# Kernel tuning notes

Measured on AMD Instinct MI355X. Metric: run time of the kernel, lower is better.

The kernel has to match this reference:

```python
import jax, jax.numpy as jnp
import numpy as np
jax.config.update("jax_enable_x64", True)

PRIMES = [2654435761, 2246822519, 3266489917, 2028178513, 1220703125, 1610612741, 805306457, 402653189, 3674653429, 2860486313, 1073676287, 2971215073, 1500450271, 3267000013, 2654435789, 4049292737]
WINDOWS = [1, 2, 4, 8]
BUCKETS = 2000000
SIGN_BITS = 8
BOUNDARY = 2
OFFSETS = (1, 2, 3, 4, 5, 6, 7, 8)
CHUNK = 32


def layer_norm(x, w, b, eps=1e-5):
    m = jnp.mean(x, axis=-1, keepdims=True)
    v = jnp.var(x, axis=-1, keepdims=True)
    return (x - m) * jax.lax.rsqrt(v + eps) * w + b


def shift_right(tokens, off):
    T = tokens.shape[1]
    return jnp.pad(tokens, ((0, 0), (off, 0)))[:, :T]


def hash_scale(tokens, window):
    # rolling polynomial hash: XOR of prime-multiplied shifted tokens
    h = jnp.zeros_like(tokens)
    for i in range(window):
        off = i + 1
        if off >= tokens.shape[1]:
            continue
        h = h ^ (shift_right(tokens, off) * PRIMES[i % len(PRIMES)])
    return h % BUCKETS


def tiny_scan(x, gw, gb, iw, ib, ow, ob, lnw, lnb):
    # chunked cumsum-based linear recurrence h_t = a_t * h_{t-1} + (1-a_t) * u_t
    B, T, D = x.shape
    S = gw.shape[0]
    K = min(CHUNK, T)
    g = jax.nn.sigmoid(jnp.einsum('btd,sd->bts', x, gw) + gb)
    drive = (1.0 - g) * (jnp.einsum('btd,sd->bts', x, iw) + ib)
    nC = T // K  # T chosen divisible by CHUNK
    a = g.reshape(B, nC, K, S)
    b = drive.reshape(B, nC, K, S)
    log_a = jnp.log(jnp.maximum(a, 1e-6))
    cum_a = jnp.exp(jnp.cumsum(log_a, axis=2))             # [B,nC,K,S]
    inv_cum_a = 1.0 / jnp.maximum(cum_a, 1e-8)
    cum_wb = jnp.cumsum(b * inv_cum_a, axis=2)

    def step(h, cs):
        ca, cw = cs                                        # [B,K,S]
        out = ca * (h[:, None, :] + cw)
        return out[:, -1], out

    h0 = jnp.zeros((B, S), x.dtype)
    _, outs = jax.lax.scan(step, h0, (jnp.swapaxes(cum_a, 0, 1), jnp.swapaxes(cum_wb, 0, 1)))
    states = jnp.swapaxes(outs, 0, 1).reshape(B, T, S)
    y = jnp.einsum('bts,ds->btd', states, ow) + ob
    return layer_norm(x + y, lnw, lnb)


def forward(chars, byte_embed, table0, table1, table2, table3, cond_w, conv_w, conv_b,
            gate_w, gate_b, inpr_w, inpr_b, outpr_w, outpr_b, scan_ln_w, scan_ln_b,
            inp_w, inp_b, r_w1, r_w2, r_proj, r_ln_w, r_ln_b, out_w, out_b):
    tokens = chars.astype(jnp.int64)
    B, T = tokens.shape
    tables = [table0, table1, table2, table3]
    keys = [hash_scale(tokens, WINDOWS[s]) for s in range(4)]
    short = [tables[s][keys[s]] for s in range(BOUNDARY)]     # each [B,T,2]
    # condition long-scale keys on sign bits of short-scale features
    cond_logits = jnp.einsum('btd,sd->bts', jnp.concatenate(short, axis=-1), cond_w)
    bits = (cond_logits > 0).astype(jnp.int64)                # [B,T,8]
    cond_key = jnp.zeros((B, T), dtype=jnp.int64)
    for i in range(SIGN_BITS):
        cond_key = cond_key ^ (bits[..., i] * PRIMES[i])
    longe = [tables[s][(keys[s] ^ cond_key) % BUCKETS] for s in range(BOUNDARY, 4)]
    hash_feat = jnp.concatenate(short + longe, axis=-1)       # [B,T,8]
    # causal depthwise conv over hash features
    C = hash_feat.shape[-1]
    ht = jnp.swapaxes(hash_feat, 1, 2)                        # [B,C,T]
    Kc = conv_w.shape[-1]
    conv = jax.lax.conv_general_dilated(ht, conv_w, (1,), [(Kc - 1, 0)],
                                        dimension_numbers=('NCH', 'OIH', 'NCH'),
                                        feature_group_count=C)
    hash_feat = jax.nn.silu(jnp.swapaxes(conv + conv_b[None, :, None], 1, 2))
    byte_emb = byte_embed[tokens]                             # [B,T,64]
    # match features: equality with k-shifted sequence
    mfs = []
    for k in OFFSETS:
        m = (tokens == shift_right(tokens, k)).astype(jnp.float32)
        m = m.at[:, :k].set(0.0)
        mfs.append(m)
    mf = jnp.stack(mfs, axis=-1)                              # [B,T,8]
    h = jnp.concatenate([byte_emb, hash_feat, mf], axis=-1)   # [B,T,80]
    h = tiny_scan(h, gate_w, gate_b, inpr_w, inpr_b, outpr_w, outpr_b, scan_ln_w, scan_ln_b)
    h = jax.nn.silu(jnp.einsum('btd,hd->bth', h, inp_w) + inp_b)   # [B,T,256]
    hh = jnp.einsum('bth,dh->btd',
                    jax.nn.silu(jnp.einsum('btd,hd->bth', h, r_w1)) * jnp.einsum('btd,hd->bth', h, r_w2),
                    r_proj)
    h = layer_norm(hh + h, r_ln_w, r_ln_b)
    return jnp.einsum('bth,vh->btv', h, out_w) + out_b        # [B,T,1024]


def setup_inputs() -> dict:
    key = jax.random.key(0)
    ks = jax.random.split(key, 32)
    f32 = jnp.float32
    B, T, V, EB, S, D, H = 32, 2048, 1024, 64, 32, 80, 256

    def rn(k, shape, std):
        return jax.random.normal(k, shape, dtype=f32) * std

    return {
        'chars': jax.random.randint(ks[0], (B, T), 0, V, dtype=jnp.int64),
        'byte_embed': rn(ks[1], (V, EB), 0.02),
        'table0': rn(ks[2], (BUCKETS, 2), 0.02),
        'table1': rn(ks[3], (BUCKETS, 2), 0.02),
        'table2': rn(ks[4], (BUCKETS, 2), 0.02),
        'table3': rn(ks[5], (BUCKETS, 2), 0.02),
        'cond_w': rn(ks[6], (SIGN_BITS, 2 * BOUNDARY), 0.3),
        'conv_w': rn(ks[7], (8, 1, 8), 0.2),
        'conv_b': rn(ks[8], (8,), 0.02),
        'gate_w': rn(ks[9], (S, D), 0.1),
        'gate_b': rn(ks[10], (S,), 0.02),
        'inpr_w': rn(ks[11], (S, D), 0.1),
        'inpr_b': rn(ks[12], (S,), 0.02),
        'outpr_w': rn(ks[13], (D, S), 0.1),
        'outpr_b': rn(ks[14], (D,), 0.02),
        'scan_ln_w': jnp.ones((D,), f32),
        'scan_ln_b': jnp.zeros((D,), f32),
        'inp_w': rn(ks[15], (H, D), 0.1),
        'inp_b': rn(ks[16], (H,), 0.02),
        'r_w1': rn(ks[17], (H, H), 0.05),
        'r_w2': rn(ks[18], (H, H), 0.05),
        'r_proj': rn(ks[19], (H, H), 0.05),
        'r_ln_w': jnp.ones((H,), f32),
        'r_ln_b': jnp.zeros((H,), f32),
        'out_w': rn(ks[20], (V, H), 0.05),
        'out_b': rn(ks[21], (V,), 0.02),
    }


def reference(chars, byte_embed, table0, table1, table2, table3, cond_w, conv_w, conv_b,
              gate_w, gate_b, inpr_w, inpr_b, outpr_w, outpr_b, scan_ln_w, scan_ln_b,
              inp_w, inp_b, r_w1, r_w2, r_proj, r_ln_w, r_ln_b, out_w, out_b):
    return forward(chars, byte_embed, table0, table1, table2, table3, cond_w, conv_w, conv_b,
                   gate_w, gate_b, inpr_w, inpr_b, outpr_w, outpr_b, scan_ln_w, scan_ln_b,
                   inp_w, inp_b, r_w1, r_w2, r_proj, r_ln_w, r_ln_b, out_w, out_b)
```

## Files before the change

kernel.cpp:

```cpp
#include <hip/hip_runtime.h>

#define BB 32
#define TT 2048
#define SS 32
#define DD 80
#define HH 256
#define VV 1024
#define EBD 64

typedef unsigned short u16;
typedef __attribute__((ext_vector_type(8))) __bf16 bf16x8;
typedef __attribute__((ext_vector_type(4))) float f32x4;

#define MFMA(a, b, c) __builtin_amdgcn_mfma_f32_16x16x32_bf16(a, b, c, 0, 0, 0)

__device__ inline u16 f2bu(float f) {
    unsigned u = __float_as_uint(f);
    return (u16)((u + 0x7FFFu + ((u >> 16) & 1u)) >> 16);
}
__device__ inline __bf16 f2b(float f) {
    u16 r = f2bu(f);
    return __builtin_bit_cast(__bf16, r);
}
__device__ inline float b2f(u16 h) { return __uint_as_float(((unsigned)h) << 16); }

__device__ inline bf16x8 ldfrag(const u16* base, int row, int k0, int lane) {
    return *(const bf16x8*)(base + (size_t)row * 256 + k0 + ((lane >> 4) << 3));
}
__device__ inline bf16x8 ldfrag96(const u16* base, int row, int k0, int lane) {
    return *(const bf16x8*)(base + (size_t)row * 96 + k0 + ((lane >> 4) << 3));
}

__global__ __launch_bounds__(256) void k_prep(const float* __restrict__ w1,
                                              const float* __restrict__ w2,
                                              const float* __restrict__ wp,
                                              const float* __restrict__ ow,
                                              const float* __restrict__ iw,
                                              u16* __restrict__ wbf) {
    int i = blockIdx.x * 256 + threadIdx.x;
    if (i >= 483328) return;
    float v;
    if (i < 65536) v = w1[i];
    else if (i < 131072) v = w2[i - 65536];
    else if (i < 196608) v = wp[i - 131072];
    else if (i < 458752) v = ow[i - 196608];
    else {
        int j = i - 458752;
        int row = j / 96, col = j % 96;
        v = (col < 80) ? iw[row * 80 + col] : 0.f;
    }
    wbf[i] = f2bu(v);
}

__global__ __launch_bounds__(256) void k_hash(const int* __restrict__ tok,
                                              const float* __restrict__ t0,
                                              const float* __restrict__ t1,
                                              const float* __restrict__ t2,
                                              const float* __restrict__ t3,
                                              const float* __restrict__ cond_w,
                                              float* __restrict__ raw) {
    int idx = blockIdx.x * 256 + threadIdx.x;
    if (idx >= BB * TT) return;
    int b = idx / TT, t = idx % TT;
    const int* tr = tok + b * TT;

    unsigned long long tv[8];
#pragma unroll
    for (int i = 0; i < 8; i++) {
        int ts = t - 1 - i;
        tv[i] = (ts >= 0) ? (unsigned long long)(unsigned)tr[ts] : 0ull;
    }
    const unsigned long long P[8] = {2654435761ull, 2246822519ull, 3266489917ull,
                                     2028178513ull, 1220703125ull, 1610612741ull,
                                     805306457ull, 402653189ull};
    unsigned long long x = 0ull;
    x ^= tv[0] * P[0]; unsigned long long k0 = x % 2000000ull;
    x ^= tv[1] * P[1]; unsigned long long k1 = x % 2000000ull;
    x ^= tv[2] * P[2]; x ^= tv[3] * P[3]; unsigned long long k2 = x % 2000000ull;
    x ^= tv[4] * P[4]; x ^= tv[5] * P[5];
    x ^= tv[6] * P[6]; x ^= tv[7] * P[7]; unsigned long long k3 = x % 2000000ull;

    float f0 = t0[k0 * 2], f1 = t0[k0 * 2 + 1];
    float f2 = t1[k1 * 2], f3 = t1[k1 * 2 + 1];

    unsigned long long ck = 0ull;
#pragma unroll
    for (int j = 0; j < 8; j++) {
        float lg = f0 * cond_w[j * 4 + 0] + f1 * cond_w[j * 4 + 1] +
                   f2 * cond_w[j * 4 + 2] + f3 * cond_w[j * 4 + 3];
        if (lg > 0.f) ck ^= P[j];
    }
    unsigned long long lk2 = (k2 ^ ck) % 2000000ull;
    unsigned long long lk3 = (k3 ^ ck) % 2000000ull;

    float* o = raw + (size_t)idx * 8;
    o[0] = f0; o[1] = f1; o[2] = f2; o[3] = f3;
    o[4] = t2[lk2 * 2]; o[5] = t2[lk2 * 2 + 1];
    o[6] = t3[lk3 * 2]; o[7] = t3[lk3 * 2 + 1];
}

__global__ __launch_bounds__(256) void k_feat(const int* __restrict__ tok,
                                              const float* __restrict__ be,
                                              const float* __restrict__ raw,
                                              const float* __restrict__ conv_w,
                                              const float* __restrict__ conv_b,
                                              float* __restrict__ hf) {
    int idx = blockIdx.x * 256 + threadIdx.x;
    if (idx >= BB * TT) return;
    int b = idx / TT, t = idx % TT;
    const int* tr = tok + b * TT;
    float* o = hf + (size_t)idx * DD;

    int tk = tr[t];
    const float* ber = be + (size_t)tk * EBD;
#pragma unroll
    for (int q = 0; q < 16; q++) *(f32x4*)(o + q * 4) = *(const f32x4*)(ber + q * 4);

#pragma unroll
    for (int c = 0; c < 8; c++) {
        float acc = conv_b[c];
#pragma unroll
        for (int k = 0; k < 8; k++) {
            int ts = t - 7 + k;
            if (ts >= 0) acc += conv_w[c * 8 + k] * raw[((size_t)(b * TT + ts)) * 8 + c];
        }
        o[64 + c] = acc / (1.f + expf(-acc));
    }

#pragma unroll
    for (int k = 1; k <= 8; k++) {
        float m = (t >= k && tk == tr[t - k]) ? 1.f : 0.f;
        o[71 + k] = m;
    }
}

__global__ __launch_bounds__(256) void k_gates(const float* __restrict__ hf,
                                               const float* __restrict__ gw,
                                               const float* __restrict__ gb,
                                               const float* __restrict__ iw,
                                               const float* __restrict__ ib,
                                               float* __restrict__ Ag,
                                               float* __restrict__ Dr) {
    __shared__ float xs[64][DD];
    __shared__ float gws[32 * 81];
    __shared__ float iws[32 * 81];
    int blk = blockIdx.x;
    int b = blk >> 5;
    int t0 = (blk & 31) << 6;
    const float* src = hf + ((size_t)(b * TT + t0)) * DD;
    for (int i = threadIdx.x; i < 64 * DD; i += 256) xs[i / DD][i % DD] = src[i];
    for (int i = threadIdx.x; i < 32 * 80; i += 256) {
        int s = i / 80, d = i % 80;
        gws[s * 81 + d] = gw[i];
        iws[s * 81 + d] = iw[i];
    }
    __syncthreads();

    for (int p = threadIdx.x; p < 64 * SS; p += 256) {
        int s = p & 31, tt = p >> 5;
        float ga = gb[s], ia = ib[s];
        for (int d = 0; d < DD; d++) {
            float xv = xs[tt][d];
            ga += xv * gws[s * 81 + d];
            ia += xv * iws[s * 81 + d];
        }
        float g = 1.f / (1.f + expf(-ga));
        float drv = (1.f - g) * ia;
        size_t oo = ((size_t)(b * SS + s)) * TT + t0 + tt;
        Ag[oo] = g;
        Dr[oo] = drv;
    }
}

__global__ __launch_bounds__(64) void k_scan_par(const float* __restrict__ Ag,
                                                 const float* __restrict__ Dr,
                                                 float* __restrict__ st) {
    int bs = blockIdx.x;
    int b = bs >> 5, s = bs & 31;
    int c = threadIdx.x;
    const float* ar = Ag + (size_t)bs * TT + c * 32;
    const float* dr = Dr + (size_t)bs * TT + c * 32;

    float ca[32], cw[32];
    float lacc = 0.f, wacc = 0.f;
#pragma unroll
    for (int k = 0; k < 32; k += 4) {
        f32x4 av = *(const f32x4*)(ar + k);
        f32x4 dv = *(const f32x4*)(dr + k);
#pragma unroll
        for (int j = 0; j < 4; j++) {
            lacc += logf(fmaxf(av[j], 1e-6f));
            float cav = expf(lacc);
            ca[k + j] = cav;
            wacc += dv[j] / fmaxf(cav, 1e-8f);
            cw[k + j] = wacc;
        }
    }

    float A = ca[31];
    float Bc = ca[31] * wacc;
    for (int off = 1; off < 64; off <<= 1) {
        float Ap = __shfl_up(A, off, 64);
        float Bp = __shfl_up(Bc, off, 64);
        if (c >= off) {
            Bc = A * Bp + Bc;
            A = A * Ap;
        }
    }
    float h0 = __shfl_up(Bc, 1, 64);
    if (c == 0) h0 = 0.f;

    float* op = st + ((size_t)(b * TT + c * 32)) * SS + s;
#pragma unroll
    for (int k = 0; k < 32; k++)
        op[(size_t)k * SS] = ca[k] * (h0 + cw[k]);
}

__global__ __launch_bounds__(256) void k_post(const float* __restrict__ st,
                                              const float* __restrict__ hf,
                                              const float* __restrict__ ow,
                                              const float* __restrict__ ob,
                                              const float* __restrict__ lnw,
                                              const float* __restrict__ lnb,
                                              u16* __restrict__ h1p) {
    __shared__ float ows[DD * SS];
    for (int i = threadIdx.x; i < DD * SS; i += 256) ows[i] = ow[i];
    __syncthreads();

    int idx = blockIdx.x * 256 + threadIdx.x;
    if (idx >= BB * TT) return;
    const float* sp = st + (size_t)idx * SS;
    float sv[SS];
#pragma unroll
    for (int i = 0; i < SS; i += 4) {
        f32x4 v4 = *(const f32x4*)(sp + i);
        sv[i] = v4[0]; sv[i + 1] = v4[1]; sv[i + 2] = v4[2]; sv[i + 3] = v4[3];
    }
    const float* x = hf + (size_t)idx * DD;

    float s1 = 0.f, s2 = 0.f;
    for (int d = 0; d < DD; d++) {
        float acc = ob[d];
#pragma unroll
        for (int i = 0; i < SS; i++) acc += sv[i] * ows[d * SS + i];
        float v = acc + x[d];
        s1 += v; s2 += v * v;
    }
    float m = s1 * (1.f / DD);
    float var = s2 * (1.f / DD) - m * m;
    float rs = rsqrtf(var + 1e-5f);
    u16* o = h1p + (size_t)idx * 96;
    for (int d = 0; d < DD; d++) {
        float acc = ob[d];
#pragma unroll
        for (int i = 0; i < SS; i++) acc += sv[i] * ows[d * SS + i];
        float v = acc + x[d];
        o[d] = f2bu((v - m) * rs * lnw[d] + lnb[d]);
    }
    *(f32x4*)(o + 80) = f32x4{0.f, 0.f, 0.f, 0.f};
    *(f32x4*)(o + 88) = f32x4{0.f, 0.f, 0.f, 0.f};
}

__global__ __launch_bounds__(256) void k_mlp1m(const u16* __restrict__ h1p,
                                               const u16* __restrict__ wb,
                                               const float* __restrict__ bias,
                                               u16* __restrict__ h2) {
    int lane = threadIdx.x & 63, wv = threadIdx.x >> 6;
    int r0 = blockIdx.x * 64;
    int c0 = wv * 64;
    f32x4 acc[4][4] = {};
#pragma unroll
    for (int ks = 0; ks < 3; ks++) {
        int k0 = ks * 32;
        bf16x8 a[4];
#pragma unroll
        for (int mi = 0; mi < 4; mi++) a[mi] = ldfrag96(h1p, r0 + mi * 16 + (lane & 15), k0, lane);
#pragma unroll
        for (int ni = 0; ni < 4; ni++) {
            bf16x8 b = ldfrag96(wb, c0 + ni * 16 + (lane & 15), k0, lane);
#pragma unroll
            for (int mi = 0; mi < 4; mi++) acc[mi][ni] = MFMA(a[mi], b, acc[mi][ni]);
        }
    }
    int g = lane >> 4, cl = lane & 15;
#pragma unroll
    for (int ni = 0; ni < 4; ni++) {
        float bv = bias[c0 + ni * 16 + cl];
#pragma unroll
        for (int mi = 0; mi < 4; mi++)
#pragma unroll
            for (int r = 0; r < 4; r++) {
                float v = acc[mi][ni][r] + bv;
                h2[(size_t)(r0 + mi * 16 + g * 4 + r) * 256 + c0 + ni * 16 + cl] =
                    f2bu(v / (1.f + expf(-v)));
            }
    }
}

__global__ __launch_bounds__(256) void k_gemm_u(const u16* __restrict__ x,
                                                const u16* __restrict__ w1,
                                                const u16* __restrict__ w2,
                                                u16* __restrict__ U) {
    int lane = threadIdx.x & 63, wv = threadIdx.x >> 6;
    int r0 = blockIdx.x * 64;
    int c0 = blockIdx.y * 128 + wv * 32;
    f32x4 a1[4][2] = {}, a2[4][2] = {};
    for (int ks = 0; ks < 8; ks++) {
        int k0 = ks * 32;
        bf16x8 a[4];
#pragma unroll
        for (int mi = 0; mi < 4; mi++) a[mi] = ldfrag(x, r0 + mi * 16 + (lane & 15), k0, lane);
#pragma unroll
        for (int ni = 0; ni < 2; ni++) {
            bf16x8 b1 = ldfrag(w1, c0 + ni * 16 + (lane & 15), k0, lane);
            bf16x8 b2 = ldfrag(w2, c0 + ni * 16 + (lane & 15), k0, lane);
#pragma unroll
            for (int mi = 0; mi < 4; mi++) {
                a1[mi][ni] = MFMA(a[mi], b1, a1[mi][ni]);
                a2[mi][ni] = MFMA(a[mi], b2, a2[mi][ni]);
            }
        }
    }
    int g = lane >> 4, cl = lane & 15;
#pragma unroll
    for (int mi = 0; mi < 4; mi++)
#pragma unroll
        for (int ni = 0; ni < 2; ni++)
#pragma unroll
            for (int r = 0; r < 4; r++) {
                float v1 = a1[mi][ni][r], v2 = a2[mi][ni][r];
                float u = v1 / (1.f + expf(-v1)) * v2;
                U[(size_t)(r0 + mi * 16 + g * 4 + r) * 256 + c0 + ni * 16 + cl] = f2bu(u);
            }
}

__global__ __launch_bounds__(256) void k_gemm_proj(const u16* __restrict__ U,
                                                   const u16* __restrict__ wp,
                                                   const u16* __restrict__ x,
                                                   const float* __restrict__ lnw,
                                                   const float* __restrict__ lnb,
                                                   u16* __restrict__ h3) {
    __shared__ float redS[64][4], redQ[64][4];
    int lane = threadIdx.x & 63, wv = threadIdx.x >> 6;
    int r0 = blockIdx.x * 64;
    int c0 = wv * 64;
    f32x4 acc[4][4] = {};
    for (int ks = 0; ks < 8; ks++) {
        int k0 = ks * 32;
        bf16x8 a[4];
#pragma unroll
        for (int mi = 0; mi < 4; mi++) a[mi] = ldfrag(U, r0 + mi * 16 + (lane & 15), k0, lane);
#pragma unroll
        for (int ni = 0; ni < 4; ni++) {
            bf16x8 b = ldfrag(wp, c0 + ni * 16 + (lane & 15), k0, lane);
#pragma unroll
            for (int mi = 0; mi < 4; mi++) acc[mi][ni] = MFMA(a[mi], b, acc[mi][ni]);
        }
    }
    int g = lane >> 4, cl = lane & 15;
#pragma unroll
    for (int mi = 0; mi < 4; mi++)
#pragma unroll
        for (int r = 0; r < 4; r++) {
            float s = 0.f, q = 0.f;
            int row = mi * 16 + g * 4 + r;
#pragma unroll
            for (int ni = 0; ni < 4; ni++) {
                int col = c0 + ni * 16 + cl;
                float v = acc[mi][ni][r] + b2f(x[(size_t)(r0 + row) * 256 + col]);
                acc[mi][ni][r] = v;
                s += v; q += v * v;
            }
            for (int m = 1; m < 16; m <<= 1) {
                s += __shfl_xor(s, m, 64);
                q += __shfl_xor(q, m, 64);
            }
            if (cl == 0) { redS[row][wv] = s; redQ[row][wv] = q; }
        }
    __syncthreads();

    float lw[4], lb[4];
#pragma unroll
    for (int ni = 0; ni < 4; ni++) {
        lw[ni] = lnw[c0 + ni * 16 + cl];
        lb[ni] = lnb[c0 + ni * 16 + cl];
    }
#pragma unroll
    for (int mi = 0; mi < 4; mi++)
#pragma unroll
        for (int r = 0; r < 4; r++) {
            int row = mi * 16 + g * 4 + r;
            float S = redS[row][0] + redS[row][1] + redS[row][2] + redS[row][3];
            float Q = redQ[row][0] + redQ[row][1] + redQ[row][2] + redQ[row][3];
            float m = S * (1.f / 256.f);
            float rs = rsqrtf(Q * (1.f / 256.f) - m * m + 1e-5f);
#pragma unroll
            for (int ni = 0; ni < 4; ni++) {
                float y = (acc[mi][ni][r] - m) * rs * lw[ni] + lb[ni];
                h3[(size_t)(r0 + row) * 256 + c0 + ni * 16 + cl] = f2bu(y);
            }
        }
}

#define SA 40
__global__ __launch_bounds__(256) void k_out3(const u16* __restrict__ h3,
                                              const u16* __restrict__ ow,
                                              const float* __restrict__ bias,
                                              float* __restrict__ out) {
    __shared__ u16 As[2][128 * SA];
    __shared__ u16 Bs[2][128 * SA];
    int tid = threadIdx.x, lane = tid & 63, wv = tid >> 6;
    int r0 = blockIdx.x * 128;
    int c0g = blockIdx.y * 128;
    int wr = (wv >> 1) * 64, wc = (wv & 1) * 64;
    int rl = lane & 15, g = lane >> 4;

    int row0_ = tid >> 2, cc0_ = tid & 3;
    int row1_ = (tid + 256) >> 2, cc1_ = tid & 3;
    bf16x8 rA0, rA1, rB0, rB1;

#define LOADT(kt)                                                                     \
    {                                                                                 \
        int kbase = (kt) * 32;                                                        \
        rA0 = *(const bf16x8*)(h3 + (size_t)(r0 + row0_) * 256 + kbase + cc0_ * 8);   \
        rA1 = *(const bf16x8*)(h3 + (size_t)(r0 + row1_) * 256 + kbase + cc1_ * 8);   \
        rB0 = *(const bf16x8*)(ow + (size_t)(c0g + row0_) * 256 + kbase + cc0_ * 8);  \
        rB1 = *(const bf16x8*)(ow + (size_t)(c0g + row1_) * 256 + kbase + cc1_ * 8);  \
    }
#define WRITET(buf)                                                                   \
    {                                                                                 \
        *(bf16x8*)&As[buf][row0_ * SA + cc0_ * 8] = rA0;                              \
        *(bf16x8*)&As[buf][row1_ * SA + cc1_ * 8] = rA1;                              \
        *(bf16x8*)&Bs[buf][row0_ * SA + cc0_ * 8] = rB0;                              \
        *(bf16x8*)&Bs[buf][row1_ * SA + cc1_ * 8] = rB1;                              \
    }

    LOADT(0);
    WRITET(0);
    f32x4 acc[4][4] = {};
    for (int kt = 0; kt < 8; kt++) {
        int buf = kt & 1;
        if (kt < 7) LOADT(kt + 1);
        __syncthreads();
        bf16x8 a[4], b[4];
#pragma unroll
        for (int mi = 0; mi < 4; mi++) a[mi] = *(const bf16x8*)&As[buf][(wr + mi * 16 + rl) * SA + g * 8];
#pragma unroll
        for (int ni = 0; ni < 4; ni++) b[ni] = *(const bf16x8*)&Bs[buf][(wc + ni * 16 + rl) * SA + g * 8];
#pragma unroll
        for (int ni = 0; ni < 4; ni++)
#pragma unroll
            for (int mi = 0; mi < 4; mi++) acc[mi][ni] = MFMA(a[mi], b[ni], acc[mi][ni]);
        if (kt < 7) WRITET(buf ^ 1);
    }
#undef LOADT
#undef WRITET

    int cl = lane & 15;
#pragma unroll
    for (int ni = 0; ni < 4; ni++) {
        float bv = bias[c0g + wc + ni * 16 + cl];
#pragma unroll
        for (int mi = 0; mi < 4; mi++)
#pragma unroll
            for (int r = 0; r < 4; r++)
                out[(size_t)(r0 + wr + mi * 16 + g * 4 + r) * VV + c0g + wc + ni * 16 + cl] =
                    acc[mi][ni][r] + bv;
    }
}

extern "C" void kernel_launch(void* const* d_in, const int* in_sizes, int n_in,
                              void* d_out, int out_size, void* d_ws, size_t ws_size,
                              hipStream_t stream) {
    const int* chars        = (const int*)d_in[0];
    const float* byte_embed = (const float*)d_in[1];
    const float* table0     = (const float*)d_in[2];
    const float* table1     = (const float*)d_in[3];
    const float* table2     = (const float*)d_in[4];
    const float* table3     = (const float*)d_in[5];
    const float* cond_w     = (const float*)d_in[6];
    const float* conv_w     = (const float*)d_in[7];
    const float* conv_b     = (const float*)d_in[8];
    const float* gate_w     = (const float*)d_in[9];
    const float* gate_b     = (const float*)d_in[10];
    const float* inpr_w     = (const float*)d_in[11];
    const float* inpr_b     = (const float*)d_in[12];
    const float* outpr_w    = (const float*)d_in[13];
    const float* outpr_b    = (const float*)d_in[14];
    const float* scan_ln_w  = (const float*)d_in[15];
    const float* scan_ln_b  = (const float*)d_in[16];
    const float* inp_w      = (const float*)d_in[17];
    const float* inp_b      = (const float*)d_in[18];
    const float* r_w1       = (const float*)d_in[19];
    const float* r_w2       = (const float*)d_in[20];
    const float* r_proj     = (const float*)d_in[21];
    const float* r_ln_w     = (const float*)d_in[22];
    const float* r_ln_b     = (const float*)d_in[23];
    const float* out_w      = (const float*)d_in[24];
    const float* out_b      = (const float*)d_in[25];

    char* ws = (char*)d_ws;
    u16*   wbf = (u16*)(ws + 0);
    u16*   w1b = wbf;
    u16*   w2b = wbf + 65536;
    u16*   wpb = wbf + 131072;
    u16*   owb = wbf + 196608;
    u16*   iwb = wbf + 458752;
    float* hf  = (float*)(ws + 1048576);
    float* raw = (float*)(ws + 24117248);
    float* Ag  = (float*)(ws + 24117248);
    float* Dr  = (float*)(ws + 32505856);
    float* st  = (float*)(ws + 40894464);
    u16*   h1p = (u16*)(ws + 49283072);
    u16*   h2b = (u16*)(ws + 1048576);
    u16*   Ub  = (u16*)(ws + 34603008);
    u16*   h3b = (u16*)(ws + 34603008);
    float* out = (float*)d_out;

    k_prep <<<1888, 256, 0, stream>>>(r_w1, r_w2, r_proj, out_w, inp_w, wbf);
    k_hash <<<256, 256, 0, stream>>>(chars, table0, table1, table2, table3, cond_w, raw);
    k_feat <<<256, 256, 0, stream>>>(chars, byte_embed, raw, conv_w, conv_b, hf);
    k_gates<<<1024, 256, 0, stream>>>(hf, gate_w, gate_b, inpr_w, inpr_b, Ag, Dr);
    k_scan_par<<<1024, 64, 0, stream>>>(Ag, Dr, st);
    k_post <<<256, 256, 0, stream>>>(st, hf, outpr_w, outpr_b, scan_ln_w, scan_ln_b, h1p);
    k_mlp1m<<<1024, 256, 0, stream>>>(h1p, iwb, inp_b, h2b);
    k_gemm_u   <<<dim3(1024, 2), 256, 0, stream>>>(h2b, w1b, w2b, Ub);
    k_gemm_proj<<<1024, 256, 0, stream>>>(Ub, wpb, h2b, r_ln_w, r_ln_b, h3b);
    k_out3     <<<dim3(512, 8), 256, 0, stream>>>(h3b, owb, out_b, out);
}
```

Before: 381.6 us.

## Fuse three MLP GEMMs into one kernel via LDS, loop output column groups

Merges the input projection, the gated SwiGLU GEMM and the projection+residual+layernorm kernel into one kernel per 64-row tile. Intermediates stay in shared memory instead of round-tripping through global memory. The output GEMM now loops over all 8 column groups inside each block instead of using a 2D grid, so the h3 tile is reused from cache. The cost is more LDS per block (about 68KB), which may lower occupancy, and the output grid shrinks to 512 blocks, each running longer.

```diff
diff --git a/kernel.cpp b/kernel.cpp
--- a/kernel.cpp
+++ b/kernel.cpp
@@ -261,149 +261,150 @@
     *(f32x4*)(o + 88) = f32x4{0.f, 0.f, 0.f, 0.f};
 }
 
-__global__ __launch_bounds__(256) void k_mlp1m(const u16* __restrict__ h1p,
-                                               const u16* __restrict__ wb,
-                                               const float* __restrict__ bias,
-                                               u16* __restrict__ h2) {
-    int lane = threadIdx.x & 63, wv = threadIdx.x >> 6;
-    int r0 = blockIdx.x * 64;
-    int c0 = wv * 64;
-    f32x4 acc[4][4] = {};
-#pragma unroll
-    for (int ks = 0; ks < 3; ks++) {
-        int k0 = ks * 32;
-        bf16x8 a[4];
-#pragma unroll
-        for (int mi = 0; mi < 4; mi++) a[mi] = ldfrag96(h1p, r0 + mi * 16 + (lane & 15), k0, lane);
-#pragma unroll
-        for (int ni = 0; ni < 4; ni++) {
-            bf16x8 b = ldfrag96(wb, c0 + ni * 16 + (lane & 15), k0, lane);
-#pragma unroll
-            for (int mi = 0; mi < 4; mi++) acc[mi][ni] = MFMA(a[mi], b, acc[mi][ni]);
-        }
-    }
-    int g = lane >> 4, cl = lane & 15;
-#pragma unroll
-    for (int ni = 0; ni < 4; ni++) {
-        float bv = bias[c0 + ni * 16 + cl];
-#pragma unroll
-        for (int mi = 0; mi < 4; mi++)
-#pragma unroll
-            for (int r = 0; r < 4; r++) {
-                float v = acc[mi][ni][r] + bv;
-                h2[(size_t)(r0 + mi * 16 + g * 4 + r) * 256 + c0 + ni * 16 + cl] =
-                    f2bu(v / (1.f + expf(-v)));
-            }
-    }
-}
-
-__global__ __launch_bounds__(256) void k_gemm_u(const u16* __restrict__ x,
+#define SX 264
+__global__ __launch_bounds__(256) void k_gmlp_f(const u16* __restrict__ h1p,
+                                                const u16* __restrict__ iwb,
+                                                const float* __restrict__ ibias,
                                                 const u16* __restrict__ w1,
                                                 const u16* __restrict__ w2,
-                                                u16* __restrict__ U) {
-    int lane = threadIdx.x & 63, wv = threadIdx.x >> 6;
-    int r0 = blockIdx.x * 64;
-    int c0 = blockIdx.y * 128 + wv * 32;
-    f32x4 a1[4][2] = {}, a2[4][2] = {};
-    for (int ks = 0; ks < 8; ks++) {
-        int k0 = ks * 32;
-        bf16x8 a[4];
-#pragma unroll
-        for (int mi = 0; mi < 4; mi++) a[mi] = ldfrag(x, r0 + mi * 16 + (lane & 15), k0, lane);
-#pragma unroll
-        for (int ni = 0; ni < 2; ni++) {
-            bf16x8 b1 = ldfrag(w1, c0 + ni * 16 + (lane & 15), k0, lane);
-            bf16x8 b2 = ldfrag(w2, c0 + ni * 16 + (lane & 15), k0, lane);
-#pragma unroll
-            for (int mi = 0; mi < 4; mi++) {
-                a1[mi][ni] = MFMA(a[mi], b1, a1[mi][ni]);
-                a2[mi][ni] = MFMA(a[mi], b2, a2[mi][ni]);
-            }
-        }
-    }
-    int g = lane >> 4, cl = lane & 15;
-#pragma unroll
-    for (int mi = 0; mi < 4; mi++)
-#pragma unroll
-        for (int ni = 0; ni < 2; ni++)
-#pragma unroll
-            for (int r = 0; r < 4; r++) {
-                float v1 = a1[mi][ni][r], v2 = a2[mi][ni][r];
-                float u = v1 / (1.f + expf(-v1)) * v2;
-                U[(size_t)(r0 + mi * 16 + g * 4 + r) * 256 + c0 + ni * 16 + cl] = f2bu(u);
-            }
-}
-
-__global__ __launch_bounds__(256) void k_gemm_proj(const u16* __restrict__ U,
-                                                   const u16* __restrict__ wp,
-                                                   const u16* __restrict__ x,
-                                                   const float* __restrict__ lnw,
-                                                   const float* __restrict__ lnb,
-                                                   u16* __restrict__ h3) {
+                                                const u16* __restrict__ wp,
+                                                const float* __restrict__ lnw,
+                                                const float* __restrict__ lnb,
+                                                u16* __restrict__ h3) {
+    __shared__ u16 Xs[64 * SX];
+    __shared__ u16 Us[64 * SX];
     __shared__ float redS[64][4], redQ[64][4];
     int lane = threadIdx.x & 63, wv = threadIdx.x >> 6;
     int r0 = blockIdx.x * 64;
-    int c0 = wv * 64;
-    f32x4 acc[4][4] = {};
-    for (int ks = 0; ks < 8; ks++) {
-        int k0 = ks * 32;
-        bf16x8 a[4];
-#pragma unroll
-        for (int mi = 0; mi < 4; mi++) a[mi] = ldfrag(U, r0 + mi * 16 + (lane & 15), k0, lane);
+    int g = lane >> 4, cl = lane & 15, rl = lane & 15;
+
+    {
+        int c0 = wv * 64;
+        f32x4 acc[4][4] = {};
+#pragma unroll
+        for (int ks = 0; ks < 3; ks++) {
+            int k0 = ks * 32;
+            bf16x8 a[4];
+#pragma unroll
+            for (int mi = 0; mi < 4; mi++) a[mi] = ldfrag96(h1p, r0 + mi * 16 + rl, k0, lane);
+#pragma unroll
+            for (int ni = 0; ni < 4; ni++) {
+                bf16x8 b = ldfrag96(iwb, c0 + ni * 16 + rl, k0, lane);
+#pragma unroll
+                for (int mi = 0; mi < 4; mi++) acc[mi][ni] = MFMA(a[mi], b, acc[mi][ni]);
+            }
+        }
 #pragma unroll
         for (int ni = 0; ni < 4; ni++) {
-            bf16x8 b = ldfrag(wp, c0 + ni * 16 + (lane & 15), k0, lane);
-#pragma unroll
-            for (int mi = 0; mi < 4; mi++) acc[mi][ni] = MFMA(a[mi], b, acc[mi][ni]);
-        }
-    }
-    int g = lane >> 4, cl = lane & 15;
-#pragma unroll
-    for (int mi = 0; mi < 4; mi++)
-#pragma unroll
-        for (int r = 0; r < 4; r++) {
-            float s = 0.f, q = 0.f;
-            int row = mi * 16 + g * 4 + r;
+            float bv = ibias[c0 + ni * 16 + cl];
+#pragma unroll
+            for (int mi = 0; mi < 4; mi++)
+#pragma unroll
+                for (int r = 0; r < 4; r++) {
+                    float v = acc[mi][ni][r] + bv;
+                    Xs[(mi * 16 + g * 4 + r) * SX + c0 + ni * 16 + cl] =
+                        f2bu(v / (1.f + expf(-v)));
+                }
+        }
+    }
+    __syncthreads();
+
+    for (int cg = 0; cg < 2; cg++) {
+        int c0 = cg * 128 + wv * 32;
+        f32x4 a1[4][2] = {}, a2[4][2] = {};
+        for (int ks = 0; ks < 8; ks++) {
+            int k0 = ks * 32 + (g << 3);
+            bf16x8 a[4];
+#pragma unroll
+            for (int mi = 0; mi < 4; mi++)
+                a[mi] = *(const bf16x8*)&Xs[(mi * 16 + rl) * SX + k0];
+#pragma unroll
+            for (int ni = 0; ni < 2; ni++) {
+                bf16x8 b1 = ldfrag(w1, c0 + ni * 16 + rl, ks * 32, lane);
+                bf16x8 b2 = ldfrag(w2, c0 + ni * 16 + rl, ks * 32, lane);
+#pragma unroll
+                for (int mi = 0; mi < 4; mi++) {
+                    a1[mi][ni] = MFMA(a[mi], b1, a1[mi][ni]);
+                    a2[mi][ni] = MFMA(a[mi], b2, a2[mi][ni]);
+                }
+            }
+        }
+#pragma unroll
+        for (int mi = 0; mi < 4; mi++)
+#pragma unroll
+            for (int ni = 0; ni < 2; ni++)
+#pragma unroll
+                for (int r = 0; r < 4; r++) {
+                    float v1 = a1[mi][ni][r], v2 = a2[mi][ni][r];
+                    float u = v1 / (1.f + expf(-v1)) * v2;
+                    Us[(mi * 16 + g * 4 + r) * SX + c0 + ni * 16 + cl] = f2bu(u);
+                }
+    }
+    __syncthreads();
+
+    {
+        int c0 = wv * 64;
+        f32x4 acc[4][4] = {};
+        for (int ks = 0; ks < 8; ks++) {
+            int k0 = ks * 32 + (g << 3);
+            bf16x8 a[4];
+#pragma unroll
+            for (int mi = 0; mi < 4; mi++)
+                a[mi] = *(const bf16x8*)&Us[(mi * 16 + rl) * SX + k0];
 #pragma unroll
             for (int ni = 0; ni < 4; ni++) {
-                int col = c0 + ni * 16 + cl;
-                float v = acc[mi][ni][r] + b2f(x[(size_t)(r0 + row) * 256 + col]);
-                acc[mi][ni][r] = v;
-                s += v; q += v * v;
+                bf16x8 b = ldfrag(wp, c0 + ni * 16 + rl, ks * 32, lane);
+#pragma unroll
+                for (int mi = 0; mi < 4; mi++) acc[mi][ni] = MFMA(a[mi], b, acc[mi][ni]);
             }
-            for (int m = 1; m < 16; m <<= 1) {
-                s += __shfl_xor(s, m, 64);
-                q += __shfl_xor(q, m, 64);
+        }
+#pragma unroll
+        for (int mi = 0; mi < 4; mi++)
+#pragma unroll
+            for (int r = 0; r < 4; r++) {
+                float s = 0.f, q = 0.f;
+                int row = mi * 16 + g * 4 + r;
+#pragma unroll
+                for (int ni = 0; ni < 4; ni++) {
+                    int col = c0 + ni * 16 + cl;
+                    float v = acc[mi][ni][r] + b2f(Xs[row * SX + col]);
+                    acc[mi][ni][r] = v;
+                    s += v; q += v * v;
+                }
+                for (int m = 1; m < 16; m <<= 1) {
+                    s += __shfl_xor(s, m, 64);
+                    q += __shfl_xor(q, m, 64);
+                }
+                if (cl == 0) { redS[row][wv] = s; redQ[row][wv] = q; }
             }
-            if (cl == 0) { redS[row][wv] = s; redQ[row][wv] = q; }
-        }
-    __syncthreads();
-
-    float lw[4], lb[4];
-#pragma unroll
-    for (int ni = 0; ni < 4; ni++) {
-        lw[ni] = lnw[c0 + ni * 16 + cl];
-        lb[ni] = lnb[c0 + ni * 16 + cl];
-    }
-#pragma unroll
-    for (int mi = 0; mi < 4; mi++)
-#pragma unroll
-        for (int r = 0; r < 4; r++) {
-            int row = mi * 16 + g * 4 + r;
-            float S = redS[row][0] + redS[row][1] + redS[row][2] + redS[row][3];
-            float Q = redQ[row][0] + redQ[row][1] + redQ[row][2] + redQ[row][3];
-            float m = S * (1.f / 256.f);
-            float rs = rsqrtf(Q * (1.f / 256.f) - m * m + 1e-5f);
-#pragma unroll
-            for (int ni = 0; ni < 4; ni++) {
-                float y = (acc[mi][ni][r] - m) * rs * lw[ni] + lb[ni];
-                h3[(size_t)(r0 + row) * 256 + c0 + ni * 16 + cl] = f2bu(y);
+        __syncthreads();
+
+        float lw[4], lb[4];
+#pragma unroll
+        for (int ni = 0; ni < 4; ni++) {
+            lw[ni] = lnw[c0 + ni * 16 + cl];
+            lb[ni] = lnb[c0 + ni * 16 + cl];
+        }
+#pragma unroll
+        for (int mi = 0; mi < 4; mi++)
+#pragma unroll
+            for (int r = 0; r < 4; r++) {
+                int row = mi * 16 + g * 4 + r;
+                float S = redS[row][0] + redS[row][1] + redS[row][2] + redS[row][3];
+                float Q = redQ[row][0] + redQ[row][1] + redQ[row][2] + redQ[row][3];
+                float m = S * (1.f / 256.f);
+                float rs = rsqrtf(Q * (1.f / 256.f) - m * m + 1e-5f);
+#pragma unroll
+                for (int ni = 0; ni < 4; ni++) {
+                    float y = (acc[mi][ni][r] - m) * rs * lw[ni] + lb[ni];
+                    h3[(size_t)(r0 + row) * 256 + c0 + ni * 16 + cl] = f2bu(y);
+                }
             }
-        }
+    }
 }
 
 #define SA 40
-__global__ __launch_bounds__(256) void k_out3(const u16* __restrict__ h3,
+__global__ __launch_bounds__(256) void k_out4(const u16* __restrict__ h3,
                                               const u16* __restrict__ ow,
                                               const float* __restrict__ bias,
                                               float* __restrict__ out) {
@@ -411,7 +412,6 @@
     __shared__ u16 Bs[2][128 * SA];
     int tid = threadIdx.x, lane = tid & 63, wv = tid >> 6;
     int r0 = blockIdx.x * 128;
-    int c0g = blockIdx.y * 128;
     int wr = (wv >> 1) * 64, wc = (wv & 1) * 64;
     int rl = lane & 15, g = lane >> 4;
 
@@ -419,54 +419,60 @@
     int row1_ = (tid + 256) >> 2, cc1_ = tid & 3;
     bf16x8 rA0, rA1, rB0, rB1;
 
-#define LOADT(kt)                                                                     \
-    {                                                                                 \
-        int kbase = (kt) * 32;                                                        \
-        rA0 = *(const bf16x8*)(h3 + (size_t)(r0 + row0_) * 256 + kbase + cc0_ * 8);   \
-        rA1 = *(const bf16x8*)(h3 + (size_t)(r0 + row1_) * 256 + kbase + cc1_ * 8);   \
-        rB0 = *(const bf16x8*)(ow + (size_t)(c0g + row0_) * 256 + kbase + cc0_ * 8);  \
-        rB1 = *(const bf16x8*)(ow + (size_t)(c0g + row1_) * 256 + kbase + cc1_ * 8);  \
-    }
-#define WRITET(buf)                                                                   \
-    {                                                                                 \
-        *(bf16x8*)&As[buf][row0_ * SA + cc0_ * 8] = rA0;                              \
-        *(bf16x8*)&As[buf][row1_ * SA + cc1_ * 8] = rA1;                              \
-        *(bf16x8*)&Bs[buf][row0_ * SA + cc0_ * 8] = rB0;                              \
-        *(bf16x8*)&Bs[buf][row1_ * SA + cc1_ * 8] = rB1;                              \
-    }
-
-    LOADT(0);
-    WRITET(0);
-    f32x4 acc[4][4] = {};
-    for (int kt = 0; kt < 8; kt++) {
-        int buf = kt & 1;
-        if (kt < 7) LOADT(kt + 1);
+#define LOADT(cg, kt)                                                                      \
+    {                                                                                      \
+        int kbase = (kt) * 32;                                                             \
+        int c0g = (cg) * 128;                                                              \
+        rA0 = *(const bf16x8*)(h3 + (size_t)(r0 + row0_) * 256 + kbase + cc0_ * 8);        \
+        rA1 = *(const bf16x8*)(h3 + (size_t)(r0 + row1_) * 256 + kbase + cc1_ * 8);        \
+        rB0 = *(const bf16x8*)(ow + (size_t)(c0g + row0_) * 256 + kbase + cc0_ * 8);       \
+        rB1 = *(const bf16x8*)(ow + (size_t)(c0g + row1_) * 256 + kbase + cc1_ * 8);       \
+    }
+#define WRITET(buf)                                                                        \
+    {                                                                                      \
+        *(bf16x8*)&As[buf][row0_ * SA + cc0_ * 8] = rA0;                                   \
+        *(bf16x8*)&As[buf][row1_ * SA + cc1_ * 8] = rA1;                                   \
+        *(bf16x8*)&Bs[buf][row0_ * SA + cc0_ * 8] = rB0;                                   \
+        *(bf16x8*)&Bs[buf][row1_ * SA + cc1_ * 8] = rB1;                                   \
+    }
+
+    for (int cg = 0; cg < 8; cg++) {
+        LOADT(cg, 0);
+        WRITET(0);
+        f32x4 acc[4][4] = {};
+        for (int kt = 0; kt < 8; kt++) {
+            int buf = kt & 1;
+            if (kt < 7) LOADT(cg, kt + 1);
+            __syncthreads();
+            bf16x8 a[4], b[4];
+#pragma unroll
+            for (int mi = 0; mi < 4; mi++)
+                a[mi] = *(const bf16x8*)&As[buf][(wr + mi * 16 + rl) * SA + g * 8];
+#pragma unroll
+            for (int ni = 0; ni < 4; ni++)
+                b[ni] = *(const bf16x8*)&Bs[buf][(wc + ni * 16 + rl) * SA + g * 8];
+#pragma unroll
+            for (int ni = 0; ni < 4; ni++)
+#pragma unroll
+                for (int mi = 0; mi < 4; mi++) acc[mi][ni] = MFMA(a[mi], b[ni], acc[mi][ni]);
+            if (kt < 7) WRITET(buf ^ 1);
+        }
+        int c0g = cg * 128;
+        int cl = lane & 15;
+#pragma unroll
+        for (int ni = 0; ni < 4; ni++) {
+            float bv = bias[c0g + wc + ni * 16 + cl];
+#pragma unroll
+            for (int mi = 0; mi < 4; mi++)
+#pragma unroll
+                for (int r = 0; r < 4; r++)
+                    out[(size_t)(r0 + wr + mi * 16 + g * 4 + r) * VV + c0g + wc + ni * 16 + cl] =
+                        acc[mi][ni][r] + bv;
+        }
         __syncthreads();
-        bf16x8 a[4], b[4];
-#pragma unroll
-        for (int mi = 0; mi < 4; mi++) a[mi] = *(const bf16x8*)&As[buf][(wr + mi * 16 + rl) * SA + g * 8];
-#pragma unroll
-        for (int ni = 0; ni < 4; ni++) b[ni] = *(const bf16x8*)&Bs[buf][(wc + ni * 16 + rl) * SA + g * 8];
-#pragma unroll
-        for (int ni = 0; ni < 4; ni++)
-#pragma unroll
-            for (int mi = 0; mi < 4; mi++) acc[mi][ni] = MFMA(a[mi], b[ni], acc[mi][ni]);
-        if (kt < 7) WRITET(buf ^ 1);
     }
 #undef LOADT
 #undef WRITET
-
-    int cl = lane & 15;
-#pragma unroll
-    for (int ni = 0; ni < 4; ni++) {
-        float bv = bias[c0g + wc + ni * 16 + cl];
-#pragma unroll
-        for (int mi = 0; mi < 4; mi++)
-#pragma unroll
-            for (int r = 0; r < 4; r++)
-                out[(size_t)(r0 + wr + mi * 16 + g * 4 + r) * VV + c0g + wc + ni * 16 + cl] =
-                    acc[mi][ni][r] + bv;
-    }
 }
 
 extern "C" void kernel_launch(void* const* d_in, const int* in_sizes, int n_in,
@@ -512,9 +518,7 @@
     float* Dr  = (float*)(ws + 32505856);
     float* st  = (float*)(ws + 40894464);
     u16*   h1p = (u16*)(ws + 49283072);
-    u16*   h2b = (u16*)(ws + 1048576);
-    u16*   Ub  = (u16*)(ws + 34603008);
-    u16*   h3b = (u16*)(ws + 34603008);
+    u16*   h3b = (u16*)(ws + 1048576);
     float* out = (float*)d_out;
 
     k_prep <<<1888, 256, 0, stream>>>(r_w1, r_w2, r_proj, out_w, inp_w, wbf);
@@ -523,8 +527,6 @@
     k_gates<<<1024, 256, 0, stream>>>(hf, gate_w, gate_b, inpr_w, inpr_b, Ag, Dr);
     k_scan_par<<<1024, 64, 0, stream>>>(Ag, Dr, st);
     k_post <<<256, 256, 0, stream>>>(st, hf, outpr_w, outpr_b, scan_ln_w, scan_ln_b, h1p);
-    k_mlp1m<<<1024, 256, 0, stream>>>(h1p, iwb, inp_b, h2b);
-    k_gemm_u   <<<dim3(1024, 2), 256, 0, stream>>>(h2b, w1b, w2b, Ub);
-    k_gemm_proj<<<1024, 256, 0, stream>>>(Ub, wpb, h2b, r_ln_w, r_ln_b, h3b);
-    k_out3     <<<dim3(512, 8), 256, 0, stream>>>(h3b, owb, out_b, out);
-}
+    k_gmlp_f<<<1024, 256, 0, stream>>>(h1p, iwb, inp_b, w1b, w2b, wpb, r_ln_w, r_ln_b, h3b);
+    k_out4 <<<512, 256, 0, stream>>>(h3b, owb, out_b, out);
+}
```

Result: faster. 339.7 us (-11.0%).
